# Optimization experiments

Hardware: AMD Instinct MI355X
Metric: run time of the kernel (lower is better)

Reference implementation:

```python
import jax, jax.numpy as jnp
import numpy as np

HEADS = 4
DIM_HEAD = 32
DIM = 128
B, N, Hq, Wg = 2, 6, 32, 32   # batch, cameras, BEV grid
HK, WK = 28, 60               # image feature map


def _ln(x, g, b, eps=1e-5):
    mu = jnp.mean(x, axis=-1, keepdims=True)
    var = jnp.mean((x - mu) ** 2, axis=-1, keepdims=True)
    return (x - mu) * jax.lax.rsqrt(var + eps) * g + b


def setup_inputs() -> dict:
    key = jax.random.key(0)
    ks = jax.random.split(key, 12)
    s = 0.05  # weight scale to keep softmax logits well-conditioned
    inp = {
        'q': jax.random.normal(ks[0], (B, N, DIM, Hq, Wg), jnp.float32),
        'k': jax.random.normal(ks[1], (B, N, DIM, HK, WK), jnp.float32),
        'v': jax.random.normal(ks[2], (B, N, DIM, HK, WK), jnp.float32),
        'skip': jax.random.normal(ks[3], (B, DIM, Hq, Wg), jnp.float32),
        'q_ln_g': jnp.ones((DIM,), jnp.float32),
        'q_ln_b': jnp.zeros((DIM,), jnp.float32),
        'Wq': s * jax.random.normal(ks[4], (DIM, HEADS * DIM_HEAD), jnp.float32),
        'bq': jnp.zeros((HEADS * DIM_HEAD,), jnp.float32),
        'k_ln_g': jnp.ones((DIM,), jnp.float32),
        'k_ln_b': jnp.zeros((DIM,), jnp.float32),
        'Wk': s * jax.random.normal(ks[5], (DIM, HEADS * DIM_HEAD), jnp.float32),
        'bk': jnp.zeros((HEADS * DIM_HEAD,), jnp.float32),
        'v_ln_g': jnp.ones((DIM,), jnp.float32),
        'v_ln_b': jnp.zeros((DIM,), jnp.float32),
        'Wv': s * jax.random.normal(ks[6], (DIM, HEADS * DIM_HEAD), jnp.float32),
        'bv': jnp.zeros((HEADS * DIM_HEAD,), jnp.float32),
        'Wp': s * jax.random.normal(ks[7], (HEADS * DIM_HEAD, DIM), jnp.float32),
        'bp': jnp.zeros((DIM,), jnp.float32),
        'pre_g': jnp.ones((DIM,), jnp.float32),
        'pre_b': jnp.zeros((DIM,), jnp.float32),
        'W1': s * jax.random.normal(ks[8], (DIM, 2 * DIM), jnp.float32),
        'b1': jnp.zeros((2 * DIM,), jnp.float32),
        'W2': s * jax.random.normal(ks[9], (2 * DIM, DIM), jnp.float32),
        'b2': jnp.zeros((DIM,), jnp.float32),
        'post_g': jnp.ones((DIM,), jnp.float32),
        'post_b': jnp.zeros((DIM,), jnp.float32),
    }
    return inp


def reference(q, k, v, skip, q_ln_g, q_ln_b, Wq, bq, k_ln_g, k_ln_b, Wk, bk,
              v_ln_g, v_ln_b, Wv, bv, Wp, bp, pre_g, pre_b,
              W1, b1, W2, b2, post_g, post_b):
    b, n, d, H, W = q.shape
    Q = H * W
    K = k.shape[3] * k.shape[4]
    m, dh = HEADS, DIM_HEAD
    # b n d H W -> b n Q d   /  b n d h w -> b n K d  /  b (n K) d
    qf = q.transpose(0, 1, 3, 4, 2).reshape(b, n, Q, d)
    kf = k.transpose(0, 1, 3, 4, 2).reshape(b, n, K, d)
    vf = v.transpose(0, 1, 3, 4, 2).reshape(b, n * K, d)
    # norm -> linear, then split heads: b ... (m dh) -> (b m) ... dh
    qh = (_ln(qf, q_ln_g, q_ln_b) @ Wq + bq).reshape(b, n, Q, m, dh)
    qh = qh.transpose(0, 3, 1, 2, 4).reshape(b * m, n, Q, dh)
    kh = (_ln(kf, k_ln_g, k_ln_b) @ Wk + bk).reshape(b, n, K, m, dh)
    kh = kh.transpose(0, 3, 1, 2, 4).reshape(b * m, n, K, dh)
    vh = (_ln(vf, v_ln_g, v_ln_b) @ Wv + bv).reshape(b, n * K, m, dh)
    vh = vh.transpose(0, 2, 1, 3).reshape(b * m, n * K, dh)
    scale = dh ** -0.5
    dot = scale * jnp.einsum('anqd,ankd->anqk', qh, kh)   # (b m) n Q K
    dot = dot.transpose(0, 2, 1, 3).reshape(b * m, Q, n * K)  # fold views into keys
    att = jax.nn.softmax(dot, axis=-1)
    a = jnp.einsum('aqk,akd->aqd', att, vh)               # (b m) Q dh
    a = a.reshape(b, m, Q, dh).transpose(0, 2, 1, 3).reshape(b, Q, m * dh)
    z = a @ Wp + bp
    z = z + skip.transpose(0, 2, 3, 1).reshape(b, Q, d)
    z = _ln(z, pre_g, pre_b)
    z = z + (jax.nn.gelu(z @ W1 + b1, approximate=False) @ W2 + b2)
    z = _ln(z, post_g, post_b)
    return z.reshape(b, H, W, d).transpose(0, 3, 1, 2)
```

## Files before the change

kernel.cpp:

```cpp
#include <hip/hip_runtime.h>
#include <math.h>

#define NCAM 6
#define BSZ 2
#define SQL 1024
#define SKL 1680
#define NHEAD 4
#define DHEAD 32
#define QSCALE 0.25503494f

typedef unsigned short ushort_t;
typedef unsigned int uint_t;
typedef __attribute__((ext_vector_type(8))) short short8;
typedef __attribute__((ext_vector_type(4))) float f32x4;

#define MFMA16 __builtin_amdgcn_mfma_f32_16x16x32_bf16

__device__ __forceinline__ ushort_t f2bf(float x) {
  uint_t u = __builtin_bit_cast(uint_t, x);
  u += 0x7FFFu + ((u >> 16) & 1u);
  return (ushort_t)(u >> 16);
}

__device__ __forceinline__ float fast_gelu(float x) {
  const float ax = fabsf(x) * 0.70710678118654752f;
  const float tt = __builtin_amdgcn_rcpf(fmaf(0.3275911f, ax, 1.f));
  float poly = fmaf(tt, 1.061405429f, -1.453152027f);
  poly = fmaf(tt, poly, 1.421413741f);
  poly = fmaf(tt, poly, -0.284496736f);
  poly = fmaf(tt, poly, 0.254829592f);
  poly *= tt;
  const float e = __builtin_amdgcn_exp2f(-ax * ax * 1.4426950408889634f);
  float er = fmaf(-poly, e, 1.f);
  er = copysignf(er, x);
  return 0.5f * x * (1.f + er);
}

__global__ __launch_bounds__(256) void prep_kernel(
    const float* __restrict__ Wq, const float* __restrict__ qg, const float* __restrict__ qb, const float* __restrict__ bq,
    const float* __restrict__ Wk, const float* __restrict__ kg, const float* __restrict__ kbb, const float* __restrict__ bk,
    const float* __restrict__ Wv, const float* __restrict__ vg, const float* __restrict__ vbb, const float* __restrict__ bv,
    const float* __restrict__ Wp,
    const float* __restrict__ W1, const float* __restrict__ pre_g, const float* __restrict__ pre_b, const float* __restrict__ b1,
    const float* __restrict__ W2,
    ushort_t* WqT, ushort_t* WkT, ushort_t* WvT, ushort_t* WpT, ushort_t* W1T, ushort_t* W2T,
    float* uq, float* bbq, float* uk, float* bbk, float* uv, float* bbv, float* b1p) {
  const int mb = blockIdx.x;
  const float *W, *g = nullptr, *bln = nullptr, *bias = nullptr;
  ushort_t* WT; float *u = nullptr, *bb = nullptr;
  int kin = 128, nout = 128, ob;
  if (mb < 4)       { W=Wq; g=qg; bln=qb;   bias=bq; WT=WqT; u=uq; bb=bbq; ob=mb*32; }
  else if (mb < 8)  { W=Wk; g=kg; bln=kbb;  bias=bk; WT=WkT; u=uk; bb=bbk; ob=(mb-4)*32; }
  else if (mb < 12) { W=Wv; g=vg; bln=vbb;  bias=bv; WT=WvT; u=uv; bb=bbv; ob=(mb-8)*32; }
  else if (mb < 16) { W=Wp; WT=WpT; ob=(mb-12)*32; }
  else if (mb < 24) { W=W1; g=pre_g; bln=pre_b; bias=b1; WT=W1T; bb=b1p; nout=256; ob=(mb-16)*32; }
  else              { W=W2; WT=W2T; kin=256; ob=(mb-24)*32; }
  const int t = threadIdx.x;
  const int oc = t & 31, ig = t >> 5;
  const int out = ob + oc;
  const int nper = kin >> 3;
  float su = 0.f, sb = 0.f;
  for (int j = 0; j < nper; ++j) {
    const int in = ig * nper + j;
    const float wv_ = W[(size_t)in * nout + out];
    const float wg = g ? g[in] * wv_ : wv_;
    WT[(size_t)out * kin + in] = f2bf(wg);
    su += wg;
    if (bln) sb += bln[in] * wv_;
  }
  __shared__ float sU[8][32], sB[8][32];
  sU[ig][oc] = su; sB[ig][oc] = sb;
  __syncthreads();
  if (t < 32) {
    float tu = 0.f, tb = 0.f;
#pragma unroll
    for (int i = 0; i < 8; ++i) { tu += sU[i][t]; tb += sB[i][t]; }
    if (u)  u[ob + t] = tu;
    if (bb) bb[ob + t] = tb + (bias ? bias[ob + t] : 0.f);
  }
}

__global__ __launch_bounds__(256) void proj_mfma(
    const float* __restrict__ xq, const float* __restrict__ xk, const float* __restrict__ xv,
    const ushort_t* __restrict__ WqT, const ushort_t* __restrict__ WkT, const ushort_t* __restrict__ WvT,
    const float* __restrict__ uq, const float* __restrict__ uk, const float* __restrict__ uv,
    const float* __restrict__ bbq, const float* __restrict__ bbk, const float* __restrict__ bbv,
    ushort_t* __restrict__ Qh, ushort_t* __restrict__ Kh, ushort_t* __restrict__ Vt) {
  int blk = blockIdx.x;
  const float* x; const ushort_t* WT; const float* u; const float* bb;
  ushort_t* out; int S, ntile, vmode; float oscale;
  if (blk < 192)      { x=xq; WT=WqT; u=uq; bb=bbq; out=Qh; S=SQL; ntile=16; vmode=0; oscale=QSCALE; }
  else if (blk < 516) { blk-=192; x=xk; WT=WkT; u=uk; bb=bbk; out=Kh; S=SKL; ntile=27; vmode=0; oscale=1.f; }
  else                { blk-=516; x=xv; WT=WvT; u=uv; bb=bbv; out=Vt; S=SKL; ntile=27; vmode=1; oscale=1.f; }
  const int bn = blk / ntile;
  const int pos0 = (blk - bn * ntile) * 64;
  int valid = S - pos0; if (valid > 64) valid = 64;

  const int t = threadIdx.x;
  __shared__ ushort_t sX[64 * 128];
  __shared__ float sS1[4][64], sS2[4][64];
  __shared__ float sMu[64], sRs[64];

  {
    const int pos = t & 63, qr = t >> 6;
    int lp = pos; if (lp >= valid) lp = valid - 1;
    const float* xb = x + ((size_t)bn * 128 + qr * 32) * S + pos0 + lp;
    float v[32]; float s1 = 0.f, s2 = 0.f;
#pragma unroll
    for (int j = 0; j < 32; ++j) { float xv_ = xb[(size_t)j * S]; v[j] = xv_; s1 += xv_; s2 += xv_ * xv_; }
    sS1[qr][pos] = s1; sS2[qr][pos] = s2;
#pragma unroll
    for (int c = 0; c < 4; ++c) {
      short8 pk;
#pragma unroll
      for (int e = 0; e < 8; ++e) pk[e] = (short)f2bf(v[c * 8 + e]);
      const int phys = (qr * 4 + c) ^ (pos & 7);
      *((short8*)&sX[pos * 128 + phys * 8]) = pk;
    }
  }
  __syncthreads();
  if (t < 64) {
    const float a1 = sS1[0][t] + sS1[1][t] + sS1[2][t] + sS1[3][t];
    const float a2 = sS2[0][t] + sS2[1][t] + sS2[2][t] + sS2[3][t];
    const float mu = a1 * (1.f / 128.f);
    sMu[t] = mu; sRs[t] = rsqrtf(a2 * (1.f / 128.f) - mu * mu + 1e-5f);
  }
  __syncthreads();

  const int w = t >> 6, l = t & 63, lq = l & 15, quad = l >> 4;
  short8 af[2][4];
#pragma unroll
  for (int ms = 0; ms < 2; ++ms)
#pragma unroll
    for (int kk = 0; kk < 4; ++kk)
      af[ms][kk] = *((const short8*)(WT + (size_t)(w * 32 + ms * 16 + lq) * 128 + quad * 8 + kk * 32));
  f32x4 acc[4][2];
#pragma unroll
  for (int ns = 0; ns < 4; ++ns)
#pragma unroll
    for (int ms = 0; ms < 2; ++ms) acc[ns][ms] = (f32x4){0.f, 0.f, 0.f, 0.f};
#pragma unroll
  for (int ns = 0; ns < 4; ++ns) {
    short8 bf[4];
#pragma unroll
    for (int kk = 0; kk < 4; ++kk) {
      const int phys = (quad + 4 * kk) ^ (lq & 7);
      bf[kk] = *((const short8*)&sX[(ns * 16 + lq) * 128 + phys * 8]);
    }
#pragma unroll
    for (int ms = 0; ms < 2; ++ms) {
      f32x4 a = acc[ns][ms];
#pragma unroll
      for (int kk = 0; kk < 4; ++kk) a = MFMA16(af[ms][kk], bf[kk], a, 0, 0, 0);
      acc[ns][ms] = a;
    }
  }

  const int b_ = bn / NCAM, cam = bn - b_ * NCAM;
  const size_t slab = (size_t)((b_ * NHEAD + w) * NCAM + cam);
#pragma unroll
  for (int ms = 0; ms < 2; ++ms) {
    float uu[4], bv_[4];
#pragma unroll
    for (int r = 0; r < 4; ++r) {
      const int og = w * 32 + ms * 16 + quad * 4 + r;
      uu[r] = u[og]; bv_[r] = bb[og];
    }
#pragma unroll
    for (int ns = 0; ns < 4; ++ns) {
      const int p = ns * 16 + lq;
      if (p < valid) {
        const float mu = sMu[p], rs = sRs[p];
        float val[4];
#pragma unroll
        for (int r = 0; r < 4; ++r)
          val[r] = ((acc[ns][ms][r] - mu * uu[r]) * rs + bv_[r]) * oscale;
        if (vmode == 0) {
          ushort_t e0 = f2bf(val[0]), e1 = f2bf(val[1]), e2 = f2bf(val[2]), e3 = f2bf(val[3]);
          ushort_t* orow = out + (slab * S + pos0 + p) * 32 + ms * 16 + quad * 4;
          *((uint_t*)orow) = (uint_t)e0 | ((uint_t)e1 << 16);
          *((uint_t*)(orow + 2)) = (uint_t)e2 | ((uint_t)e3 << 16);
        } else {
#pragma unroll
          for (int r = 0; r < 4; ++r)
            out[(slab * 32 + ms * 16 + quad * 4 + r) * (size_t)SKL + pos0 + p] = f2bf(val[r]);
        }
      }
    }
  }
}

__global__ __launch_bounds__(1024, 4) void attn_mfma(
    const ushort_t* __restrict__ Qh, const ushort_t* __restrict__ Kh,
    const ushort_t* __restrict__ Vt, ushort_t* __restrict__ Ab) {
  const int t = threadIdx.x;
  const int w = t >> 6, l = t & 63;
  const int lq = l & 15, quad = l >> 4;
  const int bm = blockIdx.x & 7;
  const int qg = w >> 3;
  const int q0 = (blockIdx.x >> 3) * 32 + qg * 16;
  const int kgrp = w & 7;
  const int camg = kgrp >> 2, kq = kgrp & 3;
  const int kstart = kq * 448;
  const int nfull = (kq == 3) ? 5 : 7;

  __shared__ ushort_t sP[16][16][72];
  __shared__ float sO[16][16][36];
  __shared__ float sL[16][16];

  f32x4 o0 = {0.f, 0.f, 0.f, 0.f};
  f32x4 o1 = {0.f, 0.f, 0.f, 0.f};
  float l_cur = 0.f;

  for (int nc = 0; nc < 3; ++nc) {
    const int n = camg * 3 + nc;
    const ushort_t* Kb = Kh + (size_t)(bm * NCAM + n) * SKL * 32;
    const ushort_t* Vb = Vt + (size_t)(bm * NCAM + n) * 32 * SKL;
    const short8 qf = *((const short8*)(Qh + ((size_t)(bm * NCAM + n) * SQL + q0 + lq) * 32 + quad * 8));

    for (int kt = 0; kt < nfull; ++kt) {
      const int kb = kstart + kt * 64;
      short8 kf[4];
#pragma unroll
      for (int st = 0; st < 4; ++st)
        kf[st] = *((const short8*)(Kb + (size_t)(kb + st * 16 + lq) * 32 + quad * 8));
      const short8 v00 = *((const short8*)(Vb + (size_t)lq * SKL + kb + quad * 8));
      const short8 v01 = *((const short8*)(Vb + (size_t)lq * SKL + kb + 32 + quad * 8));
      const short8 v10 = *((const short8*)(Vb + (size_t)(16 + lq) * SKL + kb + quad * 8));
      const short8 v11 = *((const short8*)(Vb + (size_t)(16 + lq) * SKL + kb + 32 + quad * 8));

      f32x4 s[4];
#pragma unroll
      for (int st = 0; st < 4; ++st) {
        f32x4 z = {0.f, 0.f, 0.f, 0.f};
        s[st] = MFMA16(kf[st], qf, z, 0, 0, 0);
      }
      float ls = 0.f;
#pragma unroll
      for (int st = 0; st < 4; ++st) {
        const float p0 = __builtin_amdgcn_exp2f(s[st][0]);
        const float p1 = __builtin_amdgcn_exp2f(s[st][1]);
        const float p2 = __builtin_amdgcn_exp2f(s[st][2]);
        const float p3 = __builtin_amdgcn_exp2f(s[st][3]);
        ls += (p0 + p1) + (p2 + p3);
        const uint_t pa = __builtin_amdgcn_perm(__builtin_bit_cast(uint_t, p1), __builtin_bit_cast(uint_t, p0), 0x07060302u);
        const uint_t pb = __builtin_amdgcn_perm(__builtin_bit_cast(uint_t, p3), __builtin_bit_cast(uint_t, p2), 0x07060302u);
        *((uint2*)&sP[w][lq][st * 16 + quad * 4]) = make_uint2(pa, pb);
      }
      const short8 pf0 = *((const short8*)&sP[w][lq][quad * 8]);
      const short8 pf1 = *((const short8*)&sP[w][lq][32 + quad * 8]);
      o0 = MFMA16(v00, pf0, o0, 0, 0, 0);
      o1 = MFMA16(v10, pf0, o1, 0, 0, 0);
      o0 = MFMA16(v01, pf1, o0, 0, 0, 0);
      o1 = MFMA16(v11, pf1, o1, 0, 0, 0);
      ls += __shfl_xor(ls, 16, 64);
      ls += __shfl_xor(ls, 32, 64);
      l_cur += ls;
    }

    if (kq == 3) {
      const int kb = kstart + 320;
      const short8 kf = *((const short8*)(Kb + (size_t)(kb + lq) * 32 + quad * 8));
      const short8 v00 = *((const short8*)(Vb + (size_t)lq * SKL + kb + quad * 8));
      const short8 v10 = *((const short8*)(Vb + (size_t)(16 + lq) * SKL + kb + quad * 8));
      f32x4 z = {0.f, 0.f, 0.f, 0.f};
      const f32x4 s0 = MFMA16(kf, qf, z, 0, 0, 0);
      const float p0 = __builtin_amdgcn_exp2f(s0[0]);
      const float p1 = __builtin_amdgcn_exp2f(s0[1]);
      const float p2 = __builtin_amdgcn_exp2f(s0[2]);
      const float p3 = __builtin_amdgcn_exp2f(s0[3]);
      float ls = (p0 + p1) + (p2 + p3);
      const uint_t pa = __builtin_amdgcn_perm(__builtin_bit_cast(uint_t, p1), __builtin_bit_cast(uint_t, p0), 0x07060302u);
      const uint_t pb = __builtin_amdgcn_perm(__builtin_bit_cast(uint_t, p3), __builtin_bit_cast(uint_t, p2), 0x07060302u);
      *((uint2*)&sP[w][lq][quad * 4]) = make_uint2(pa, pb);
      *((uint2*)&sP[w][lq][16 + quad * 4]) = make_uint2(0u, 0u);
      const short8 pf0 = *((const short8*)&sP[w][lq][quad * 8]);
      o0 = MFMA16(v00, pf0, o0, 0, 0, 0);
      o1 = MFMA16(v10, pf0, o1, 0, 0, 0);
      ls += __shfl_xor(ls, 16, 64);
      ls += __shfl_xor(ls, 32, 64);
      l_cur += ls;
    }
  }

  *((f32x4*)&sO[w][lq][quad * 4]) = o0;
  *((f32x4*)&sO[w][lq][16 + quad * 4]) = o1;
  if (l < 16) sL[w][l] = l_cur;
  __syncthreads();
  if (kgrp == 0) {
    float lf = 0.f;
    f32x4 a0 = {0.f, 0.f, 0.f, 0.f}, a1 = {0.f, 0.f, 0.f, 0.f};
#pragma unroll
    for (int w2 = 0; w2 < 8; ++w2) {
      const int ww = qg * 8 + w2;
      lf += sL[ww][lq];
      a0 += *((const f32x4*)&sO[ww][lq][quad * 4]);
      a1 += *((const f32x4*)&sO[ww][lq][16 + quad * 4]);
    }
    const float inv = 1.f / lf;
    const int b = bm >> 2, hm = bm & 3;
    ushort_t* op = Ab + ((size_t)b * SQL + q0 + lq) * 128 + hm * 32 + quad * 4;
    ushort4 w0 = make_ushort4(f2bf(a0[0] * inv), f2bf(a0[1] * inv), f2bf(a0[2] * inv), f2bf(a0[3] * inv));
    ushort4 w1 = make_ushort4(f2bf(a1[0] * inv), f2bf(a1[1] * inv), f2bf(a1[2] * inv), f2bf(a1[3] * inv));
    *((ushort4*)op) = w0;
    *((ushort4*)(op + 16)) = w1;
  }
}

__global__ __launch_bounds__(256) void post_mfma(
    const ushort_t* __restrict__ Ab, const float* __restrict__ skip,
    const ushort_t* __restrict__ WpT, const float* __restrict__ bp,
    const float* __restrict__ pre_g, const float* __restrict__ pre_b,
    const ushort_t* __restrict__ W1T, const float* __restrict__ b1p,
    const ushort_t* __restrict__ W2T, const float* __restrict__ b2,
    const float* __restrict__ post_g, const float* __restrict__ post_b,
    float* __restrict__ out) {
  const int t = threadIdx.x;
  const int w = t >> 6, l = t & 63, lq = l & 15, quad = l >> 4;
  const int b = blockIdx.x >> 6;
  const int p0 = (blockIdx.x & 63) * 16;

  __shared__ float zf[16 * 132];
  __shared__ float sRes[16 * 132];
  __shared__ ushort_t sZb[16 * 128];
  __shared__ ushort_t sH[16 * 256];
  __shared__ float sMu[16], sRs[16];

  f32x4 z[2] = {{0.f,0.f,0.f,0.f},{0.f,0.f,0.f,0.f}};
#pragma unroll
  for (int kk = 0; kk < 4; ++kk) {
    const short8 bfr = *((const short8*)(Ab + ((size_t)b * SQL + p0 + lq) * 128 + quad * 8 + kk * 32));
#pragma unroll
    for (int ms = 0; ms < 2; ++ms) {
      const short8 afr = *((const short8*)(WpT + (size_t)(w * 32 + ms * 16 + lq) * 128 + quad * 8 + kk * 32));
      z[ms] = MFMA16(afr, bfr, z[ms], 0, 0, 0);
    }
  }
#pragma unroll
  for (int ms = 0; ms < 2; ++ms)
#pragma unroll
    for (int r = 0; r < 4; ++r) {
      const int o = w * 32 + ms * 16 + quad * 4 + r;
      zf[lq * 132 + o] = z[ms][r] + bp[o] + skip[(size_t)b * 131072 + (size_t)o * 1024 + p0 + lq];
    }
  __syncthreads();
  if (w == 0) {
    const int pos = l & 15, qr = l >> 4;
    float s1 = 0.f, s2 = 0.f;
#pragma unroll
    for (int j = 0; j < 32; ++j) { const float vv = zf[pos * 132 + qr * 32 + j]; s1 += vv; s2 += vv * vv; }
    s1 += __shfl_xor(s1, 16, 64); s1 += __shfl_xor(s1, 32, 64);
    s2 += __shfl_xor(s2, 16, 64); s2 += __shfl_xor(s2, 32, 64);
    const float mu = s1 * (1.f / 128.f);
    if (qr == 0) { sMu[pos] = mu; sRs[pos] = rsqrtf(s2 * (1.f / 128.f) - mu * mu + 1e-5f); }
  }
  __syncthreads();
  {
    const int pos = t & 15, grp = t >> 4;
    const float mu = sMu[pos], rs = sRs[pos];
    short8 pk;
#pragma unroll
    for (int i = 0; i < 8; ++i) {
      const int ch = grp * 8 + i;
      const float nv = (zf[pos * 132 + ch] - mu) * rs;
      pk[i] = (short)f2bf(nv);
      sRes[pos * 132 + ch] = nv * pre_g[ch] + pre_b[ch];
    }
    *((short8*)&sZb[pos * 128 + (grp ^ (pos & 7)) * 8]) = pk;
  }
  __syncthreads();
  f32x4 h[4];
#pragma unroll
  for (int ms = 0; ms < 4; ++ms) h[ms] = (f32x4){0.f, 0.f, 0.f, 0.f};
  short8 bz[4];
#pragma unroll
  for (int kk = 0; kk < 4; ++kk)
    bz[kk] = *((const short8*)&sZb[lq * 128 + ((quad + 4 * kk) ^ (lq & 7)) * 8]);
#pragma unroll
  for (int ms = 0; ms < 4; ++ms)
#pragma unroll
    for (int kk = 0; kk < 4; ++kk) {
      const short8 afr = *((const short8*)(W1T + (size_t)(w * 64 + ms * 16 + lq) * 128 + quad * 8 + kk * 32));
      h[ms] = MFMA16(afr, bz[kk], h[ms], 0, 0, 0);
    }
#pragma unroll
  for (int ms = 0; ms < 4; ++ms)
#pragma unroll
    for (int r = 0; r < 4; ++r) {
      const int o = w * 64 + ms * 16 + quad * 4 + r;
      const float hv = fast_gelu(h[ms][r] + b1p[o]);
      const int phys = (o >> 3) ^ (lq & 7);
      sH[lq * 256 + phys * 8 + (o & 7)] = f2bf(hv);
    }
  __syncthreads();
  f32x4 z2[2] = {{0.f,0.f,0.f,0.f},{0.f,0.f,0.f,0.f}};
#pragma unroll
  for (int kk = 0; kk < 8; ++kk) {
    const short8 bh = *((const short8*)&sH[lq * 256 + ((quad + 4 * kk) ^ (lq & 7)) * 8]);
#pragma unroll
    for (int ms = 0; ms < 2; ++ms) {
      const short8 afr = *((const short8*)(W2T + (size_t)(w * 32 + ms * 16 + lq) * 256 + quad * 8 + kk * 32));
      z2[ms] = MFMA16(afr, bh, z2[ms], 0, 0, 0);
    }
  }
  __syncthreads();
#pragma unroll
  for (int ms = 0; ms < 2; ++ms)
#pragma unroll
    for (int r = 0; r < 4; ++r) {
      const int o = w * 32 + ms * 16 + quad * 4 + r;
      zf[lq * 132 + o] = z2[ms][r] + b2[o] + sRes[lq * 132 + o];
    }
  __syncthreads();
  if (w == 0) {
    const int pos = l & 15, qr = l >> 4;
    float s1 = 0.f, s2 = 0.f;
#pragma unroll
    for (int j = 0; j < 32; ++j) { const float vv = zf[pos * 132 + qr * 32 + j]; s1 += vv; s2 += vv * vv; }
    s1 += __shfl_xor(s1, 16, 64); s1 += __shfl_xor(s1, 32, 64);
    s2 += __shfl_xor(s2, 16, 64); s2 += __shfl_xor(s2, 32, 64);
    const float mu = s1 * (1.f / 128.f);
    if (qr == 0) { sMu[pos] = mu; sRs[pos] = rsqrtf(s2 * (1.f / 128.f) - mu * mu + 1e-5f); }
  }
  __syncthreads();
  {
    const int pos = t & 15, grp = t >> 4;
    const float mu = sMu[pos], rs = sRs[pos];
#pragma unroll
    for (int i = 0; i < 8; ++i) {
      const int ch = grp * 8 + i;
      out[(size_t)b * 131072 + (size_t)ch * 1024 + p0 + pos] =
          (zf[pos * 132 + ch] - mu) * rs * post_g[ch] + post_b[ch];
    }
  }
}

extern "C" void kernel_launch(void* const* d_in, const int* in_sizes, int n_in,
                              void* d_out, int out_size, void* d_ws, size_t ws_size,
                              hipStream_t stream) {
  const float* q_in   = (const float*)d_in[0];
  const float* k_in   = (const float*)d_in[1];
  const float* v_in   = (const float*)d_in[2];
  const float* skip   = (const float*)d_in[3];
  const float* q_ln_g = (const float*)d_in[4];
  const float* q_ln_b = (const float*)d_in[5];
  const float* Wq     = (const float*)d_in[6];
  const float* bq     = (const float*)d_in[7];
  const float* k_ln_g = (const float*)d_in[8];
  const float* k_ln_b = (const float*)d_in[9];
  const float* Wk     = (const float*)d_in[10];
  const float* bk     = (const float*)d_in[11];
  const float* v_ln_g = (const float*)d_in[12];
  const float* v_ln_b = (const float*)d_in[13];
  const float* Wv     = (const float*)d_in[14];
  const float* bv     = (const float*)d_in[15];
  const float* Wp     = (const float*)d_in[16];
  const float* bp     = (const float*)d_in[17];
  const float* pre_g  = (const float*)d_in[18];
  const float* pre_b  = (const float*)d_in[19];
  const float* W1     = (const float*)d_in[20];
  const float* b1     = (const float*)d_in[21];
  const float* W2     = (const float*)d_in[22];
  const float* b2     = (const float*)d_in[23];
  const float* post_g = (const float*)d_in[24];
  const float* post_b = (const float*)d_in[25];

  char* base = (char*)d_ws;
  ushort_t* WqT = (ushort_t*)base; base += 16384 * 2;
  ushort_t* WkT = (ushort_t*)base; base += 16384 * 2;
  ushort_t* WvT = (ushort_t*)base; base += 16384 * 2;
  ushort_t* WpT = (ushort_t*)base; base += 16384 * 2;
  ushort_t* W1T = (ushort_t*)base; base += 32768 * 2;
  ushort_t* W2T = (ushort_t*)base; base += 32768 * 2;
  float* uq  = (float*)base; base += 128 * 4;
  float* bbq = (float*)base; base += 128 * 4;
  float* uk  = (float*)base; base += 128 * 4;
  float* bbk = (float*)base; base += 128 * 4;
  float* uv  = (float*)base; base += 128 * 4;
  float* bbv = (float*)base; base += 128 * 4;
  float* b1p = (float*)base; base += 256 * 4;
  base = (char*)(((size_t)base + 255) & ~(size_t)255);
  ushort_t* Qh = (ushort_t*)base; base += (size_t)1572864 * 2;
  ushort_t* Kh = (ushort_t*)base; base += (size_t)(2580480 + 4096) * 2;
  ushort_t* Vt = (ushort_t*)base; base += (size_t)(2580480 + 4096) * 2;
  ushort_t* Ab = (ushort_t*)base; base += (size_t)262144 * 2;
  float* out = (float*)d_out;

  prep_kernel<<<28, 256, 0, stream>>>(
      Wq, q_ln_g, q_ln_b, bq, Wk, k_ln_g, k_ln_b, bk, Wv, v_ln_g, v_ln_b, bv,
      Wp, W1, pre_g, pre_b, b1, W2,
      WqT, WkT, WvT, WpT, W1T, W2T, uq, bbq, uk, bbk, uv, bbv, b1p);
  proj_mfma<<<840, 256, 0, stream>>>(
      q_in, k_in, v_in, WqT, WkT, WvT, uq, uk, uv, bbq, bbk, bbv, Qh, Kh, Vt);
  attn_mfma<<<256, 1024, 0, stream>>>(Qh, Kh, Vt, Ab);
  post_mfma<<<128, 256, 0, stream>>>(
      Ab, skip, WpT, bp, pre_g, pre_b, W1T, b1p, W2T, b2, post_g, post_b, out);
}
```

Baseline: 184.5 us.

## Share K/V fragments across two query tiles per wave; vectorize projection loads

In attention, each wave now handles both 16-query tiles, so one set of K/V fragment loads feeds twice as many MFMAs. This halves the block size to 512 threads and halves redundant K/V global traffic, at the cost of more registers per wave and fewer waves for latency hiding. In the projection kernel, inputs are now read as float4 along the position axis with 8 channels per thread, and LayerNorm partial sums are spread over 16 channel groups. A no-op arithmetic tweak in the post LayerNorm variance is also included.

```diff
diff --git a/kernel.cpp b/kernel.cpp
--- a/kernel.cpp
+++ b/kernel.cpp
@@ -98,30 +98,41 @@
 
   const int t = threadIdx.x;
   __shared__ ushort_t sX[64 * 128];
-  __shared__ float sS1[4][64], sS2[4][64];
+  __shared__ float sS1[16][64], sS2[16][64];
   __shared__ float sMu[64], sRs[64];
 
   {
-    const int pos = t & 63, qr = t >> 6;
-    int lp = pos; if (lp >= valid) lp = valid - 1;
-    const float* xb = x + ((size_t)bn * 128 + qr * 32) * S + pos0 + lp;
-    float v[32]; float s1 = 0.f, s2 = 0.f;
-#pragma unroll
-    for (int j = 0; j < 32; ++j) { float xv_ = xb[(size_t)j * S]; v[j] = xv_; s1 += xv_; s2 += xv_ * xv_; }
-    sS1[qr][pos] = s1; sS2[qr][pos] = s2;
-#pragma unroll
-    for (int c = 0; c < 4; ++c) {
+    const int posq = t & 15, chg = t >> 4;
+    int lp4 = 4 * posq; if (lp4 >= valid) lp4 = valid - 4;
+    const float* xb = x + ((size_t)bn * 128 + chg * 8) * S + pos0 + lp4;
+    float v[8][4];
+#pragma unroll
+    for (int i = 0; i < 8; ++i) {
+      const float4 f = *((const float4*)(xb + (size_t)i * S));
+      v[i][0] = f.x; v[i][1] = f.y; v[i][2] = f.z; v[i][3] = f.w;
+    }
+#pragma unroll
+    for (int j = 0; j < 4; ++j) {
+      float s1 = 0.f, s2 = 0.f;
+#pragma unroll
+      for (int i = 0; i < 8; ++i) { s1 += v[i][j]; s2 += v[i][j] * v[i][j]; }
+      sS1[chg][lp4 + j] = s1; sS2[chg][lp4 + j] = s2;
+    }
+#pragma unroll
+    for (int j = 0; j < 4; ++j) {
+      const int pos = lp4 + j;
       short8 pk;
 #pragma unroll
-      for (int e = 0; e < 8; ++e) pk[e] = (short)f2bf(v[c * 8 + e]);
-      const int phys = (qr * 4 + c) ^ (pos & 7);
+      for (int i = 0; i < 8; ++i) pk[i] = (short)f2bf(v[i][j]);
+      const int phys = chg ^ (pos & 7);
       *((short8*)&sX[pos * 128 + phys * 8]) = pk;
     }
   }
   __syncthreads();
   if (t < 64) {
-    const float a1 = sS1[0][t] + sS1[1][t] + sS1[2][t] + sS1[3][t];
-    const float a2 = sS2[0][t] + sS2[1][t] + sS2[2][t] + sS2[3][t];
+    float a1 = 0.f, a2 = 0.f;
+#pragma unroll
+    for (int g = 0; g < 16; ++g) { a1 += sS1[g][t]; a2 += sS2[g][t]; }
     const float mu = a1 * (1.f / 128.f);
     sMu[t] = mu; sRs[t] = rsqrtf(a2 * (1.f / 128.f) - mu * mu + 1e-5f);
   }
@@ -190,33 +201,33 @@
   }
 }
 
-__global__ __launch_bounds__(1024, 4) void attn_mfma(
+__global__ __launch_bounds__(512, 2) void attn_mfma(
     const ushort_t* __restrict__ Qh, const ushort_t* __restrict__ Kh,
     const ushort_t* __restrict__ Vt, ushort_t* __restrict__ Ab) {
   const int t = threadIdx.x;
   const int w = t >> 6, l = t & 63;
   const int lq = l & 15, quad = l >> 4;
   const int bm = blockIdx.x & 7;
-  const int qg = w >> 3;
-  const int q0 = (blockIdx.x >> 3) * 32 + qg * 16;
-  const int kgrp = w & 7;
-  const int camg = kgrp >> 2, kq = kgrp & 3;
+  const int q0 = (blockIdx.x >> 3) * 32;
+  const int camg = w >> 2, kq = w & 3;
   const int kstart = kq * 448;
   const int nfull = (kq == 3) ? 5 : 7;
 
-  __shared__ ushort_t sP[16][16][72];
-  __shared__ float sO[16][16][36];
-  __shared__ float sL[16][16];
-
-  f32x4 o0 = {0.f, 0.f, 0.f, 0.f};
-  f32x4 o1 = {0.f, 0.f, 0.f, 0.f};
-  float l_cur = 0.f;
+  __shared__ ushort_t sP[8][2][16][72];
+  __shared__ float sO[8][2][16][36];
+  __shared__ float sL[8][2][16];
+
+  f32x4 oA0 = {0.f,0.f,0.f,0.f}, oA1 = {0.f,0.f,0.f,0.f};
+  f32x4 oB0 = {0.f,0.f,0.f,0.f}, oB1 = {0.f,0.f,0.f,0.f};
+  float lA = 0.f, lB = 0.f;
 
   for (int nc = 0; nc < 3; ++nc) {
     const int n = camg * 3 + nc;
     const ushort_t* Kb = Kh + (size_t)(bm * NCAM + n) * SKL * 32;
     const ushort_t* Vb = Vt + (size_t)(bm * NCAM + n) * 32 * SKL;
-    const short8 qf = *((const short8*)(Qh + ((size_t)(bm * NCAM + n) * SQL + q0 + lq) * 32 + quad * 8));
+    const ushort_t* Qbase = Qh + ((size_t)(bm * NCAM + n) * SQL + q0) * 32;
+    const short8 qfA = *((const short8*)(Qbase + (size_t)lq * 32 + quad * 8));
+    const short8 qfB = *((const short8*)(Qbase + (size_t)(16 + lq) * 32 + quad * 8));
 
     for (int kt = 0; kt < nfull; ++kt) {
       const int kb = kstart + kt * 64;
@@ -229,33 +240,50 @@
       const short8 v10 = *((const short8*)(Vb + (size_t)(16 + lq) * SKL + kb + quad * 8));
       const short8 v11 = *((const short8*)(Vb + (size_t)(16 + lq) * SKL + kb + 32 + quad * 8));
 
-      f32x4 s[4];
+      f32x4 sA[4], sB[4];
 #pragma unroll
       for (int st = 0; st < 4; ++st) {
         f32x4 z = {0.f, 0.f, 0.f, 0.f};
-        s[st] = MFMA16(kf[st], qf, z, 0, 0, 0);
+        sA[st] = MFMA16(kf[st], qfA, z, 0, 0, 0);
+        sB[st] = MFMA16(kf[st], qfB, z, 0, 0, 0);
       }
-      float ls = 0.f;
+      float lsA = 0.f, lsB = 0.f;
 #pragma unroll
       for (int st = 0; st < 4; ++st) {
-        const float p0 = __builtin_amdgcn_exp2f(s[st][0]);
-        const float p1 = __builtin_amdgcn_exp2f(s[st][1]);
-        const float p2 = __builtin_amdgcn_exp2f(s[st][2]);
-        const float p3 = __builtin_amdgcn_exp2f(s[st][3]);
-        ls += (p0 + p1) + (p2 + p3);
-        const uint_t pa = __builtin_amdgcn_perm(__builtin_bit_cast(uint_t, p1), __builtin_bit_cast(uint_t, p0), 0x07060302u);
-        const uint_t pb = __builtin_amdgcn_perm(__builtin_bit_cast(uint_t, p3), __builtin_bit_cast(uint_t, p2), 0x07060302u);
-        *((uint2*)&sP[w][lq][st * 16 + quad * 4]) = make_uint2(pa, pb);
+        const float a0 = __builtin_amdgcn_exp2f(sA[st][0]);
+        const float a1 = __builtin_amdgcn_exp2f(sA[st][1]);
+        const float a2 = __builtin_amdgcn_exp2f(sA[st][2]);
+        const float a3 = __builtin_amdgcn_exp2f(sA[st][3]);
+        const float b0 = __builtin_amdgcn_exp2f(sB[st][0]);
+        const float b1 = __builtin_amdgcn_exp2f(sB[st][1]);
+        const float b2 = __builtin_amdgcn_exp2f(sB[st][2]);
+        const float b3 = __builtin_amdgcn_exp2f(sB[st][3]);
+        lsA += (a0 + a1) + (a2 + a3);
+        lsB += (b0 + b1) + (b2 + b3);
+        const uint_t pa0 = __builtin_amdgcn_perm(__builtin_bit_cast(uint_t, a1), __builtin_bit_cast(uint_t, a0), 0x07060302u);
+        const uint_t pa1 = __builtin_amdgcn_perm(__builtin_bit_cast(uint_t, a3), __builtin_bit_cast(uint_t, a2), 0x07060302u);
+        const uint_t pb0 = __builtin_amdgcn_perm(__builtin_bit_cast(uint_t, b1), __builtin_bit_cast(uint_t, b0), 0x07060302u);
+        const uint_t pb1 = __builtin_amdgcn_perm(__builtin_bit_cast(uint_t, b3), __builtin_bit_cast(uint_t, b2), 0x07060302u);
+        *((uint2*)&sP[w][0][lq][st * 16 + quad * 4]) = make_uint2(pa0, pa1);
+        *((uint2*)&sP[w][1][lq][st * 16 + quad * 4]) = make_uint2(pb0, pb1);
       }
-      const short8 pf0 = *((const short8*)&sP[w][lq][quad * 8]);
-      const short8 pf1 = *((const short8*)&sP[w][lq][32 + quad * 8]);
-      o0 = MFMA16(v00, pf0, o0, 0, 0, 0);
-      o1 = MFMA16(v10, pf0, o1, 0, 0, 0);
-      o0 = MFMA16(v01, pf1, o0, 0, 0, 0);
-      o1 = MFMA16(v11, pf1, o1, 0, 0, 0);
-      ls += __shfl_xor(ls, 16, 64);
-      ls += __shfl_xor(ls, 32, 64);
-      l_cur += ls;
+      const short8 pfA0 = *((const short8*)&sP[w][0][lq][quad * 8]);
+      const short8 pfA1 = *((const short8*)&sP[w][0][lq][32 + quad * 8]);
+      const short8 pfB0 = *((const short8*)&sP[w][1][lq][quad * 8]);
+      const short8 pfB1 = *((const short8*)&sP[w][1][lq][32 + quad * 8]);
+      oA0 = MFMA16(v00, pfA0, oA0, 0, 0, 0);
+      oA1 = MFMA16(v10, pfA0, oA1, 0, 0, 0);
+      oB0 = MFMA16(v00, pfB0, oB0, 0, 0, 0);
+      oB1 = MFMA16(v10, pfB0, oB1, 0, 0, 0);
+      oA0 = MFMA16(v01, pfA1, oA0, 0, 0, 0);
+      oA1 = MFMA16(v11, pfA1, oA1, 0, 0, 0);
+      oB0 = MFMA16(v01, pfB1, oB0, 0, 0, 0);
+      oB1 = MFMA16(v11, pfB1, oB1, 0, 0, 0);
+      lsA += __shfl_xor(lsA, 16, 64);
+      lsA += __shfl_xor(lsA, 32, 64);
+      lsB += __shfl_xor(lsB, 16, 64);
+      lsB += __shfl_xor(lsB, 32, 64);
+      lA += lsA; lB += lsB;
     }
 
     if (kq == 3) {
@@ -264,42 +292,59 @@
       const short8 v00 = *((const short8*)(Vb + (size_t)lq * SKL + kb + quad * 8));
       const short8 v10 = *((const short8*)(Vb + (size_t)(16 + lq) * SKL + kb + quad * 8));
       f32x4 z = {0.f, 0.f, 0.f, 0.f};
-      const f32x4 s0 = MFMA16(kf, qf, z, 0, 0, 0);
-      const float p0 = __builtin_amdgcn_exp2f(s0[0]);
-      const float p1 = __builtin_amdgcn_exp2f(s0[1]);
-      const float p2 = __builtin_amdgcn_exp2f(s0[2]);
-      const float p3 = __builtin_amdgcn_exp2f(s0[3]);
-      float ls = (p0 + p1) + (p2 + p3);
-      const uint_t pa = __builtin_amdgcn_perm(__builtin_bit_cast(uint_t, p1), __builtin_bit_cast(uint_t, p0), 0x07060302u);
-      const uint_t pb = __builtin_amdgcn_perm(__builtin_bit_cast(uint_t, p3), __builtin_bit_cast(uint_t, p2), 0x07060302u);
-      *((uint2*)&sP[w][lq][quad * 4]) = make_uint2(pa, pb);
-      *((uint2*)&sP[w][lq][16 + quad * 4]) = make_uint2(0u, 0u);
-      const short8 pf0 = *((const short8*)&sP[w][lq][quad * 8]);
-      o0 = MFMA16(v00, pf0, o0, 0, 0, 0);
-      o1 = MFMA16(v10, pf0, o1, 0, 0, 0);
-      ls += __shfl_xor(ls, 16, 64);
-      ls += __shfl_xor(ls, 32, 64);
-      l_cur += ls;
-    }
-  }
-
-  *((f32x4*)&sO[w][lq][quad * 4]) = o0;
-  *((f32x4*)&sO[w][lq][16 + quad * 4]) = o1;
-  if (l < 16) sL[w][l] = l_cur;
-  __syncthreads();
-  if (kgrp == 0) {
+      const f32x4 s0A = MFMA16(kf, qfA, z, 0, 0, 0);
+      const f32x4 s0B = MFMA16(kf, qfB, z, 0, 0, 0);
+      const float a0 = __builtin_amdgcn_exp2f(s0A[0]);
+      const float a1 = __builtin_amdgcn_exp2f(s0A[1]);
+      const float a2 = __builtin_amdgcn_exp2f(s0A[2]);
+      const float a3 = __builtin_amdgcn_exp2f(s0A[3]);
+      const float b0 = __builtin_amdgcn_exp2f(s0B[0]);
+      const float b1 = __builtin_amdgcn_exp2f(s0B[1]);
+      const float b2 = __builtin_amdgcn_exp2f(s0B[2]);
+      const float b3 = __builtin_amdgcn_exp2f(s0B[3]);
+      float lsA = (a0 + a1) + (a2 + a3);
+      float lsB = (b0 + b1) + (b2 + b3);
+      const uint_t pa0 = __builtin_amdgcn_perm(__builtin_bit_cast(uint_t, a1), __builtin_bit_cast(uint_t, a0), 0x07060302u);
+      const uint_t pa1 = __builtin_amdgcn_perm(__builtin_bit_cast(uint_t, a3), __builtin_bit_cast(uint_t, a2), 0x07060302u);
+      const uint_t pb0 = __builtin_amdgcn_perm(__builtin_bit_cast(uint_t, b1), __builtin_bit_cast(uint_t, b0), 0x07060302u);
+      const uint_t pb1 = __builtin_amdgcn_perm(__builtin_bit_cast(uint_t, b3), __builtin_bit_cast(uint_t, b2), 0x07060302u);
+      *((uint2*)&sP[w][0][lq][quad * 4]) = make_uint2(pa0, pa1);
+      *((uint2*)&sP[w][0][lq][16 + quad * 4]) = make_uint2(0u, 0u);
+      *((uint2*)&sP[w][1][lq][quad * 4]) = make_uint2(pb0, pb1);
+      *((uint2*)&sP[w][1][lq][16 + quad * 4]) = make_uint2(0u, 0u);
+      const short8 pfA0 = *((const short8*)&sP[w][0][lq][quad * 8]);
+      const short8 pfB0 = *((const short8*)&sP[w][1][lq][quad * 8]);
+      oA0 = MFMA16(v00, pfA0, oA0, 0, 0, 0);
+      oA1 = MFMA16(v10, pfA0, oA1, 0, 0, 0);
+      oB0 = MFMA16(v00, pfB0, oB0, 0, 0, 0);
+      oB1 = MFMA16(v10, pfB0, oB1, 0, 0, 0);
+      lsA += __shfl_xor(lsA, 16, 64);
+      lsA += __shfl_xor(lsA, 32, 64);
+      lsB += __shfl_xor(lsB, 16, 64);
+      lsB += __shfl_xor(lsB, 32, 64);
+      lA += lsA; lB += lsB;
+    }
+  }
+
+  *((f32x4*)&sO[w][0][lq][quad * 4]) = oA0;
+  *((f32x4*)&sO[w][0][lq][16 + quad * 4]) = oA1;
+  *((f32x4*)&sO[w][1][lq][quad * 4]) = oB0;
+  *((f32x4*)&sO[w][1][lq][16 + quad * 4]) = oB1;
+  if (l < 16) { sL[w][0][l] = lA; sL[w][1][l] = lB; }
+  __syncthreads();
+  if (w < 2) {
+    const int frag = w;
     float lf = 0.f;
     f32x4 a0 = {0.f, 0.f, 0.f, 0.f}, a1 = {0.f, 0.f, 0.f, 0.f};
 #pragma unroll
-    for (int w2 = 0; w2 < 8; ++w2) {
-      const int ww = qg * 8 + w2;
-      lf += sL[ww][lq];
-      a0 += *((const f32x4*)&sO[ww][lq][quad * 4]);
-      a1 += *((const f32x4*)&sO[ww][lq][16 + quad * 4]);
+    for (int ww = 0; ww < 8; ++ww) {
+      lf += sL[ww][frag][lq];
+      a0 += *((const f32x4*)&sO[ww][frag][lq][quad * 4]);
+      a1 += *((const f32x4*)&sO[ww][frag][lq][16 + quad * 4]);
     }
     const float inv = 1.f / lf;
     const int b = bm >> 2, hm = bm & 3;
-    ushort_t* op = Ab + ((size_t)b * SQL + q0 + lq) * 128 + hm * 32 + quad * 4;
+    ushort_t* op = Ab + ((size_t)b * SQL + q0 + frag * 16 + lq) * 128 + hm * 32 + quad * 4;
     ushort4 w0 = make_ushort4(f2bf(a0[0] * inv), f2bf(a0[1] * inv), f2bf(a0[2] * inv), f2bf(a0[3] * inv));
     ushort4 w1 = make_ushort4(f2bf(a1[0] * inv), f2bf(a1[1] * inv), f2bf(a1[2] * inv), f2bf(a1[3] * inv));
     *((ushort4*)op) = w0;
@@ -420,7 +465,7 @@
     s1 += __shfl_xor(s1, 16, 64); s1 += __shfl_xor(s1, 32, 64);
     s2 += __shfl_xor(s2, 16, 64); s2 += __shfl_xor(s2, 32, 64);
     const float mu = s1 * (1.f / 128.f);
-    if (qr == 0) { sMu[pos] = mu; sRs[pos] = rsqrtf(s2 * (1.f / 128.f) - mu * mu + 1e-5f); }
+    if (qr == 0) { sMu[pos] = mu; sRs[pos] = rsqrtf(s2 * (1.f / 128.f) + 1e-5f - mu * mu + mu * mu - mu * mu); }
   }
   __syncthreads();
   {
@@ -492,7 +537,7 @@
       WqT, WkT, WvT, WpT, W1T, W2T, uq, bbq, uk, bbk, uv, bbv, b1p);
   proj_mfma<<<840, 256, 0, stream>>>(
       q_in, k_in, v_in, WqT, WkT, WvT, uq, uk, uv, bbq, bbk, bbv, Qh, Kh, Vt);
-  attn_mfma<<<256, 1024, 0, stream>>>(Qh, Kh, Vt, Ab);
+  attn_mfma<<<256, 512, 0, stream>>>(Qh, Kh, Vt, Ab);
   post_mfma<<<128, 256, 0, stream>>>(
       Ab, skip, WpT, bp, pre_g, pre_b, W1T, b1p, W2T, b2, post_g, post_b, out);
 }
```

Result: faster. 174.2 us (-5.6%).
